# Optimization experiments

Hardware: AMD Instinct MI355X
Metric: run time of the kernel (lower is better)

The kernel has to match this reference:

```python
import jax, jax.numpy as jnp
import numpy as np

B, H, S, D = 4, 16, 2048, 64
NEG = -9e15


def setup_inputs() -> dict:
    key = jax.random.key(0)
    kq, kk, kv = jax.random.split(key, 3)
    q = jax.random.normal(kq, (B, H, S, D), dtype=jnp.float32)
    k = jax.random.normal(kk, (B, H, S, D), dtype=jnp.float32)
    v = jax.random.normal(kv, (B, H, S, D), dtype=jnp.float32)
    # causal mask: 1 where attention allowed, 0 where masked
    mask = jnp.tril(jnp.ones((S, S), dtype=jnp.int32))[None, None]
    return {"q": q, "k": k, "v": v, "mask": mask}


def reference(q, k, v, mask):
    d_k = q.shape[-1]
    # [B,H,S,S] scores
    scores = jnp.einsum("bhqd,bhkd->bhqk", q, k) / jnp.sqrt(jnp.float32(d_k))
    scores = jnp.where(mask == 0, jnp.float32(NEG), scores)
    attn = jax.nn.softmax(scores, axis=-1)
    return jnp.einsum("bhqk,bhkd->bhqd", attn, v)
```

## Files before the change

### kernel.cpp

```cpp
#include <hip/hip_runtime.h>

#define SLEN 2048
#define DH 64
#define NH 64
#define KVB 64
#define NT 32
#define NP 16
#define NEGBIG (-1e30f)
#define SCALE 0.18033688011112042f

typedef __attribute__((ext_vector_type(8))) short bf16x8;
typedef __attribute__((ext_vector_type(8))) unsigned short u16x8;
typedef __attribute__((ext_vector_type(16))) float f32x16;
typedef __attribute__((ext_vector_type(4))) float f32x4;
typedef __attribute__((ext_vector_type(4))) unsigned int u32x4;

__device__ __forceinline__ ushort f2bf(float f) {
  union { float f; unsigned int u; } v; v.f = f;
  unsigned int r = v.u + 0x7fffu + ((v.u >> 16) & 1u);
  return (ushort)(r >> 16);
}

__device__ __forceinline__ unsigned int cvtpk(float lo, float hi2) {
  unsigned int r;
  asm("v_cvt_pk_bf16_f32 %0, %1, %2" : "=v"(r) : "v"(lo), "v"(hi2));
  return r;
}

__device__ __forceinline__ float xsumh(float x) { return x + __shfl_xor(x, 32); }

__device__ __forceinline__ void gload16(const ushort* g, ushort* l) {
  __builtin_amdgcn_global_load_lds(
      (const __attribute__((address_space(1))) void*)g,
      (__attribute__((address_space(3))) void*)l, 16, 0, 0);
}

__global__ __launch_bounds__(256) void prep_k(const float* __restrict__ Kg,
                                              ushort* __restrict__ wsK) {
  const int head = blockIdx.x, tile = blockIdx.y, tid = threadIdx.x;
  const float* src = Kg + ((size_t)head * SLEN + (size_t)tile * KVB) * DH;
  ushort* dst = wsK + ((size_t)head * NT + tile) * (KVB * DH);
#pragma unroll
  for (int i = 0; i < 2; ++i) {
    const int id = tid + i * 256;
    const int r = id >> 3, c = id & 7;
    float4 a = *reinterpret_cast<const float4*>(src + r * DH + c * 8);
    float4 b = *reinterpret_cast<const float4*>(src + r * DH + c * 8 + 4);
    u16x8 t;
    t[0] = f2bf(a.x); t[1] = f2bf(a.y); t[2] = f2bf(a.z); t[3] = f2bf(a.w);
    t[4] = f2bf(b.x); t[5] = f2bf(b.y); t[6] = f2bf(b.z); t[7] = f2bf(b.w);
    *reinterpret_cast<u16x8*>(dst + r * DH + ((c ^ (r & 7)) * 8)) = t;
  }
}

__global__ __launch_bounds__(256) void prep_v(const float* __restrict__ Vg,
                                              ushort* __restrict__ wsV) {
  __shared__ float Vl[KVB][DH + 1];
  const int head = blockIdx.x, tile = blockIdx.y, tid = threadIdx.x;
  const float* src = Vg + ((size_t)head * SLEN + (size_t)tile * KVB) * DH;
#pragma unroll
  for (int i = 0; i < 4; ++i) {
    const int n = tid + i * 256;
    const int row = n >> 4, c4 = (n & 15) << 2;
    *reinterpret_cast<float4*>(&Vl[row][c4]) =
        *reinterpret_cast<const float4*>(src + row * DH + c4);
  }
  __syncthreads();
  ushort* dst = wsV + ((size_t)head * NT + tile) * (KVB * DH);
#pragma unroll
  for (int i = 0; i < 2; ++i) {
    const int id = tid + i * 256;
    const int d = id >> 3, c = id & 7;
    u16x8 t;
#pragma unroll
    for (int j = 0; j < 8; ++j) t[j] = f2bf(Vl[c * 8 + j][d]);
    *reinterpret_cast<u16x8*>(dst + d * DH + ((c ^ (d & 7)) * 8)) = t;
  }
}

__device__ __forceinline__ void qkt(const ushort* __restrict__ Kl,
                                    const bf16x8* qf, f32x16& s0, f32x16& s1,
                                    int ql, int hi) {
  s0 = (f32x16)0.0f; s1 = (f32x16)0.0f;
  __builtin_amdgcn_s_setprio(1);
#pragma unroll
  for (int ks = 0; ks < 4; ++ks) {
    const int c = ((ks * 2 + hi) ^ (ql & 7)) * 8;
    bf16x8 kf0 = *reinterpret_cast<const bf16x8*>(Kl + ql * 64 + c);
    bf16x8 kf1 = *reinterpret_cast<const bf16x8*>(Kl + (32 + ql) * 64 + c);
    s0 = __builtin_amdgcn_mfma_f32_32x32x16_bf16(kf0, qf[ks], s0, 0, 0, 0);
    s1 = __builtin_amdgcn_mfma_f32_32x32x16_bf16(kf1, qf[ks], s1, 0, 0, 0);
  }
  __builtin_amdgcn_s_setprio(0);
}

__device__ __forceinline__ void fin(const ushort* __restrict__ Vl,
                                    f32x16& s0, f32x16& s1, f32x16& o0,
                                    f32x16& o1, f32x4& lv, int t,
                                    int tl, int q0, int ql, int hi) {
  if (t == tl) {
    const int qg = q0 + ql;
#pragma unroll
    for (int r = 0; r < 16; ++r) {
      const int kr = t * 64 + (r & 3) + 8 * (r >> 2) + 4 * hi;
      if (kr > qg)      s0[r] = NEGBIG;
      if (kr + 32 > qg) s1[r] = NEGBIG;
    }
  }

#pragma unroll
  for (int r = 0; r < 16; ++r) s0[r] = __builtin_exp2f(s0[r]);
#pragma unroll
  for (int r = 0; r < 16; ++r) s1[r] = __builtin_exp2f(s1[r]);

#pragma unroll
  for (int r = 0; r < 16; ++r) lv[r & 3] += s0[r] + s1[r];

  unsigned int pw0[8], pw1[8];
#pragma unroll
  for (int g = 0; g < 4; ++g)
#pragma unroll
    for (int j = 0; j < 2; ++j) {
      pw0[g * 2 + j] = cvtpk(s0[4 * g + 2 * j], s0[4 * g + 2 * j + 1]);
      pw1[g * 2 + j] = cvtpk(s1[4 * g + 2 * j], s1[4 * g + 2 * j + 1]);
    }

  __builtin_amdgcn_s_setprio(1);
#pragma unroll
  for (int st = 0; st < 4; ++st) {
    const unsigned int* PW = (st < 2) ? pw0 : pw1;
    const int KH = st & 1;
    const unsigned int a0 = PW[4 * KH + 0], a1 = PW[4 * KH + 1];
    const unsigned int b0 = PW[4 * KH + 2], b1 = PW[4 * KH + 3];
    const unsigned int s0w = hi ? a0 : b0, s1w = hi ? a1 : b1;
    const unsigned int r0 = __shfl_xor(s0w, 32), r1 = __shfl_xor(s1w, 32);
    const unsigned int k0 = hi ? b0 : a0, k1 = hi ? b1 : a1;
    u32x4 fu;
    fu[0] = hi ? r0 : k0; fu[1] = hi ? r1 : k1;
    fu[2] = hi ? k0 : r0; fu[3] = hi ? k1 : r1;
    const bf16x8 pf = __builtin_bit_cast(bf16x8, fu);
    const int cv = ((st * 2 + hi) ^ (ql & 7)) * 8;
    const bf16x8 vf0 = *reinterpret_cast<const bf16x8*>(Vl + ql * 64 + cv);
    const bf16x8 vf1 = *reinterpret_cast<const bf16x8*>(Vl + (32 + ql) * 64 + cv);
    o0 = __builtin_amdgcn_mfma_f32_32x32x16_bf16(vf0, pf, o0, 0, 0, 0);
    o1 = __builtin_amdgcn_mfma_f32_32x32x16_bf16(vf1, pf, o1, 0, 0, 0);
  }
  __builtin_amdgcn_s_setprio(0);
}

__device__ __forceinline__ void load_q(const float* Qh, int q0, int ql, int hi,
                                       bf16x8* qf) {
  const float* qrow = Qh + (size_t)(q0 + ql) * DH;
#pragma unroll
  for (int ks = 0; ks < 4; ++ks) {
    const int d0 = ks * 16 + hi * 8;
    float4 a = *reinterpret_cast<const float4*>(qrow + d0);
    float4 b = *reinterpret_cast<const float4*>(qrow + d0 + 4);
    bf16x8 t;
    t[0] = (short)f2bf(a.x * SCALE); t[1] = (short)f2bf(a.y * SCALE);
    t[2] = (short)f2bf(a.z * SCALE); t[3] = (short)f2bf(a.w * SCALE);
    t[4] = (short)f2bf(b.x * SCALE); t[5] = (short)f2bf(b.y * SCALE);
    t[6] = (short)f2bf(b.z * SCALE); t[7] = (short)f2bf(b.w * SCALE);
    qf[ks] = t;
  }
}

__device__ __forceinline__ void epi(float* Ow, float* Oh, const f32x16& o,
                                    float invl, int q0, int subd, int lane) {
  const int ql = lane & 31, hi = lane >> 5;
#pragma unroll
  for (int g = 0; g < 4; ++g) {
    float4 vv = make_float4(o[4 * g] * invl, o[4 * g + 1] * invl,
                            o[4 * g + 2] * invl, o[4 * g + 3] * invl);
    *reinterpret_cast<float4*>(Ow + ql * 36 + 8 * g + 4 * hi) = vv;
  }
#pragma unroll
  for (int i = 0; i < 4; ++i) {
    const int qr = (lane >> 3) + i * 8;
    const int c4 = (lane & 7) * 4;
    float4 vv = *reinterpret_cast<const float4*>(Ow + qr * 36 + c4);
    *reinterpret_cast<float4*>(Oh + (size_t)(q0 + qr) * DH + subd * 32 + c4) = vv;
  }
}

__global__ __launch_bounds__(128, 2) void attn_fwd7(
    const float* __restrict__ Qg, const ushort* __restrict__ wsK,
    const ushort* __restrict__ wsV, float* __restrict__ Og) {
  __shared__ __align__(16) float smem[8192];
  ushort* stg = (ushort*)smem;

  const int head = blockIdx.x;
  const int p    = blockIdx.y;
  const int tid  = threadIdx.x;
  const int w    = tid >> 6;
  const int lane = tid & 63;
  const int hi   = lane >> 5;
  const int ql   = lane & 31;

  const int q0A = p * 64 + w * 32;
  const int q0B = (31 - p) * 64 + w * 32;
  const int tlA = p;
  const int tlB = 31 - p;
  const int nt  = 32 - p;

  const float*  Qh    = Qg + (size_t)head * SLEN * DH;
  float*        Oh    = Og + (size_t)head * SLEN * DH;
  const ushort* kbase = wsK + (size_t)head * (NT * KVB * DH);
  const ushort* vbase = wsV + (size_t)head * (NT * KVB * DH);

#define STAGE(buf, t)                                                          \
  do {                                                                         \
    const size_t tb_ = (size_t)(t) * 4096;                                     \
    _Pragma("unroll")                                                          \
    for (int j_ = 0; j_ < 4; ++j_) {                                           \
      gload16(kbase + tb_ + j_ * 1024 + tid * 8,                               \
              stg + (buf) * 8192 + j_ * 1024 + tid * 8);                       \
      gload16(vbase + tb_ + j_ * 1024 + tid * 8,                               \
              stg + (buf) * 8192 + 4096 + j_ * 1024 + tid * 8);                \
    }                                                                          \
  } while (0)

  STAGE(0, 0);

  bf16x8 qfA[4], qfB[4];
  load_q(Qh, q0A, ql, hi, qfA);
  load_q(Qh, q0B, ql, hi, qfB);

  f32x16 oA0 = (f32x16)0.0f, oA1 = (f32x16)0.0f;
  f32x16 oB0 = (f32x16)0.0f, oB1 = (f32x16)0.0f;
  f32x4 lvA = (f32x4)0.0f, lvB = (f32x4)0.0f;

  __syncthreads();

  int cur = 0;
  for (int t = 0; t < nt; ++t) {
    if (t + 1 < nt) STAGE(cur ^ 1, t + 1);

    const ushort* Kl = stg + cur * 8192;
    const ushort* Vl = Kl + 4096;
    const bool doA = (t <= tlA);

    f32x16 sB0, sB1, sA0, sA1;
    qkt(Kl, qfB, sB0, sB1, ql, hi);
    if (doA) qkt(Kl, qfA, sA0, sA1, ql, hi);
    fin(Vl, sB0, sB1, oB0, oB1, lvB, t, tlB, q0B, ql, hi);
    if (doA) fin(Vl, sA0, sA1, oA0, oA1, lvA, t, tlA, q0A, ql, hi);

    __syncthreads();
    cur ^= 1;
  }
#undef STAGE

  const float lAs = xsumh(lvA[0] + lvA[1] + lvA[2] + lvA[3]);
  const float lBs = xsumh(lvB[0] + lvB[1] + lvB[2] + lvB[3]);

  float* Ow = smem + w * 1152;
  const float iA = 1.0f / lAs, iB = 1.0f / lBs;
  epi(Ow, Oh, oA0, iA, q0A, 0, lane);
  epi(Ow, Oh, oA1, iA, q0A, 1, lane);
  epi(Ow, Oh, oB0, iB, q0B, 0, lane);
  epi(Ow, Oh, oB1, iB, q0B, 1, lane);
}

extern "C" void kernel_launch(void* const* d_in, const int* in_sizes, int n_in,
                              void* d_out, int out_size, void* d_ws, size_t ws_size,
                              hipStream_t stream) {
  const float* q = (const float*)d_in[0];
  const float* k = (const float*)d_in[1];
  const float* v = (const float*)d_in[2];
  float* out = (float*)d_out;

  const size_t per = (size_t)NH * SLEN * DH;
  ushort* wsK = (ushort*)d_ws;
  ushort* wsV = wsK + per;

  prep_k<<<dim3(NH, NT), 256, 0, stream>>>(k, wsK);
  prep_v<<<dim3(NH, NT), 256, 0, stream>>>(v, wsV);
  attn_fwd7<<<dim3(NH, NP), 128, 0, stream>>>(q, wsK, wsV, out);
}
```

Measured before the change: 91.61 us.

## Split KV tiles across two wave pairs per block and merge partial accumulators

Each block grows from two to four waves. The two wave pairs take alternating KV tiles, so each pair processes half of the causal tile range. This is a split-K style approach. Partial O accumulators and row sums from the second pair are written to shared memory and added into the first pair, which then normalises and writes the output. The software double-buffered prefetch is replaced by loading both tiles and then synchronising, so load and compute no longer overlap inside a block. The merge also adds extra barriers and LDS traffic. Launch bounds change to 256 threads with 3 blocks per SM.

```diff
diff --git a/kernel.cpp b/kernel.cpp
--- a/kernel.cpp
+++ b/kernel.cpp
@@ -8,6 +8,7 @@
 #define NP 16
 #define NEGBIG (-1e30f)
 #define SCALE 0.18033688011112042f
+#define REGION_F 4864
 
 typedef __attribute__((ext_vector_type(8))) short bf16x8;
 typedef __attribute__((ext_vector_type(8))) unsigned short u16x8;
@@ -183,10 +184,10 @@
   }
 }
 
-__global__ __launch_bounds__(128, 2) void attn_fwd7(
+__global__ __launch_bounds__(256, 3) void attn_fwd8(
     const float* __restrict__ Qg, const ushort* __restrict__ wsK,
     const ushort* __restrict__ wsV, float* __restrict__ Og) {
-  __shared__ __align__(16) float smem[8192];
+  __shared__ __align__(16) float smem[2 * REGION_F];
   ushort* stg = (ushort*)smem;
 
   const int head = blockIdx.x;
@@ -196,32 +197,19 @@
   const int lane = tid & 63;
   const int hi   = lane >> 5;
   const int ql   = lane & 31;
-
-  const int q0A = p * 64 + w * 32;
-  const int q0B = (31 - p) * 64 + w * 32;
+  const int sel  = w & 1;
+  const int pw   = w >> 1;
+
+  const int q0A = p * 64 + sel * 32;
+  const int q0B = (31 - p) * 64 + sel * 32;
   const int tlA = p;
   const int tlB = 31 - p;
-  const int nt  = 32 - p;
 
   const float*  Qh    = Qg + (size_t)head * SLEN * DH;
   float*        Oh    = Og + (size_t)head * SLEN * DH;
   const ushort* kbase = wsK + (size_t)head * (NT * KVB * DH);
   const ushort* vbase = wsV + (size_t)head * (NT * KVB * DH);
 
-#define STAGE(buf, t)                                                          \
-  do {                                                                         \
-    const size_t tb_ = (size_t)(t) * 4096;                                     \
-    _Pragma("unroll")                                                          \
-    for (int j_ = 0; j_ < 4; ++j_) {                                           \
-      gload16(kbase + tb_ + j_ * 1024 + tid * 8,                               \
-              stg + (buf) * 8192 + j_ * 1024 + tid * 8);                       \
-      gload16(vbase + tb_ + j_ * 1024 + tid * 8,                               \
-              stg + (buf) * 8192 + 4096 + j_ * 1024 + tid * 8);                \
-    }                                                                          \
-  } while (0)
-
-  STAGE(0, 0);
-
   bf16x8 qfA[4], qfB[4];
   load_q(Qh, q0A, ql, hi, qfA);
   load_q(Qh, q0B, ql, hi, qfB);
@@ -230,36 +218,81 @@
   f32x16 oB0 = (f32x16)0.0f, oB1 = (f32x16)0.0f;
   f32x4 lvA = (f32x4)0.0f, lvB = (f32x4)0.0f;
 
+#define STAGE1(slot, t)                                                        \
+  do {                                                                         \
+    const size_t tb_ = (size_t)(t) * 4096;                                     \
+    gload16(kbase + tb_ + tid * 8,        stg + (slot) * 8192 + tid * 8);      \
+    gload16(kbase + tb_ + 2048 + tid * 8, stg + (slot) * 8192 + 2048 + tid * 8);\
+    gload16(vbase + tb_ + tid * 8,        stg + (slot) * 8192 + 4096 + tid * 8);\
+    gload16(vbase + tb_ + 2048 + tid * 8,                                      \
+            stg + (slot) * 8192 + 6144 + tid * 8);                             \
+  } while (0)
+
+  for (int g = 0; g <= tlB; g += 2) {
+    STAGE1(0, g);
+    if (g + 1 <= tlB) STAGE1(1, g + 1);
+    __syncthreads();
+
+    const int t = g + pw;
+    if (t <= tlB) {
+      const ushort* Kl = stg + pw * 8192;
+      const ushort* Vl = Kl + 4096;
+      const bool doA = (t <= tlA);
+      f32x16 sB0, sB1, sA0, sA1;
+      qkt(Kl, qfB, sB0, sB1, ql, hi);
+      if (doA) qkt(Kl, qfA, sA0, sA1, ql, hi);
+      fin(Vl, sB0, sB1, oB0, oB1, lvB, t, tlB, q0B, ql, hi);
+      if (doA) fin(Vl, sA0, sA1, oA0, oA1, lvA, t, tlA, q0A, ql, hi);
+    }
+    __syncthreads();
+  }
+#undef STAGE1
+
+  if (pw == 1) {
+    float* R = smem + sel * REGION_F;
+#define DUMP(OACC, A)                                                          \
+    _Pragma("unroll")                                                          \
+    for (int g = 0; g < 4; ++g)                                                \
+      *reinterpret_cast<float4*>(R + lane * 68 + (A) * 16 + g * 4) =           \
+          make_float4(OACC[4 * g], OACC[4 * g + 1], OACC[4 * g + 2],           \
+                      OACC[4 * g + 3]);
+    DUMP(oA0, 0); DUMP(oA1, 1); DUMP(oB0, 2); DUMP(oB1, 3);
+#undef DUMP
+    *reinterpret_cast<float4*>(R + 64 * 68 + lane * 8)     =
+        make_float4(lvA[0], lvA[1], lvA[2], lvA[3]);
+    *reinterpret_cast<float4*>(R + 64 * 68 + lane * 8 + 4) =
+        make_float4(lvB[0], lvB[1], lvB[2], lvB[3]);
+  }
   __syncthreads();
-
-  int cur = 0;
-  for (int t = 0; t < nt; ++t) {
-    if (t + 1 < nt) STAGE(cur ^ 1, t + 1);
-
-    const ushort* Kl = stg + cur * 8192;
-    const ushort* Vl = Kl + 4096;
-    const bool doA = (t <= tlA);
-
-    f32x16 sB0, sB1, sA0, sA1;
-    qkt(Kl, qfB, sB0, sB1, ql, hi);
-    if (doA) qkt(Kl, qfA, sA0, sA1, ql, hi);
-    fin(Vl, sB0, sB1, oB0, oB1, lvB, t, tlB, q0B, ql, hi);
-    if (doA) fin(Vl, sA0, sA1, oA0, oA1, lvA, t, tlA, q0A, ql, hi);
-
-    __syncthreads();
-    cur ^= 1;
-  }
-#undef STAGE
-
-  const float lAs = xsumh(lvA[0] + lvA[1] + lvA[2] + lvA[3]);
-  const float lBs = xsumh(lvB[0] + lvB[1] + lvB[2] + lvB[3]);
-
-  float* Ow = smem + w * 1152;
-  const float iA = 1.0f / lAs, iB = 1.0f / lBs;
-  epi(Ow, Oh, oA0, iA, q0A, 0, lane);
-  epi(Ow, Oh, oA1, iA, q0A, 1, lane);
-  epi(Ow, Oh, oB0, iB, q0B, 0, lane);
-  epi(Ow, Oh, oB1, iB, q0B, 1, lane);
+  if (pw == 0) {
+    const float* R = smem + sel * REGION_F;
+#define TAKE(OACC, A)                                                          \
+    _Pragma("unroll")                                                          \
+    for (int g = 0; g < 4; ++g) {                                              \
+      float4 vv = *reinterpret_cast<const float4*>(R + lane * 68 + (A) * 16 +  \
+                                                   g * 4);                     \
+      OACC[4 * g] += vv.x; OACC[4 * g + 1] += vv.y;                            \
+      OACC[4 * g + 2] += vv.z; OACC[4 * g + 3] += vv.w;                        \
+    }
+    TAKE(oA0, 0); TAKE(oA1, 1); TAKE(oB0, 2); TAKE(oB1, 3);
+#undef TAKE
+    float4 la = *reinterpret_cast<const float4*>(R + 64 * 68 + lane * 8);
+    float4 lb = *reinterpret_cast<const float4*>(R + 64 * 68 + lane * 8 + 4);
+    lvA[0] += la.x; lvA[1] += la.y; lvA[2] += la.z; lvA[3] += la.w;
+    lvB[0] += lb.x; lvB[1] += lb.y; lvB[2] += lb.z; lvB[3] += lb.w;
+  }
+  __syncthreads();
+
+  if (pw == 0) {
+    const float lAs = xsumh(lvA[0] + lvA[1] + lvA[2] + lvA[3]);
+    const float lBs = xsumh(lvB[0] + lvB[1] + lvB[2] + lvB[3]);
+    float* Ow = smem + w * 1152;
+    const float iA = 1.0f / lAs, iB = 1.0f / lBs;
+    epi(Ow, Oh, oA0, iA, q0A, 0, lane);
+    epi(Ow, Oh, oA1, iA, q0A, 1, lane);
+    epi(Ow, Oh, oB0, iB, q0B, 0, lane);
+    epi(Ow, Oh, oB1, iB, q0B, 1, lane);
+  }
 }
 
 extern "C" void kernel_launch(void* const* d_in, const int* in_sizes, int n_in,
@@ -276,5 +309,5 @@
 
   prep_k<<<dim3(NH, NT), 256, 0, stream>>>(k, wsK);
   prep_v<<<dim3(NH, NT), 256, 0, stream>>>(v, wsV);
-  attn_fwd7<<<dim3(NH, NP), 128, 0, stream>>>(q, wsK, wsV, out);
-}
+  attn_fwd8<<<dim3(NH, NP), 256, 0, stream>>>(q, wsK, wsV, out);
+}
```

Result: slower. 124.5 us (+36.0%).

## Fuse K/V prep, skip masked diagonal sub-tiles, compute row sums via MFMA

Applied to the files above, without the earlier changes.

Merges the K and V bf16 conversion kernels into one launch to cut a kernel launch. In the attention kernel, wave 0 on the diagonal tile skips the upper 32-key half entirely (QK, exp, pack and PV), and the QK loop shares K fragment loads between the A and B query blocks. Row-sum accumulation moves from per-lane VALU adds plus a cross-half shuffle to an extra MFMA against a ones vector. This adds MFMA work per tile and more live registers, which may reduce occupancy.

```diff
diff --git a/kernel.cpp b/kernel.cpp
--- a/kernel.cpp
+++ b/kernel.cpp
@@ -12,7 +12,6 @@
 typedef __attribute__((ext_vector_type(8))) short bf16x8;
 typedef __attribute__((ext_vector_type(8))) unsigned short u16x8;
 typedef __attribute__((ext_vector_type(16))) float f32x16;
-typedef __attribute__((ext_vector_type(4))) float f32x4;
 typedef __attribute__((ext_vector_type(4))) unsigned int u32x4;
 
 __device__ __forceinline__ ushort f2bf(float f) {
@@ -27,123 +26,129 @@
   return r;
 }
 
-__device__ __forceinline__ float xsumh(float x) { return x + __shfl_xor(x, 32); }
-
 __device__ __forceinline__ void gload16(const ushort* g, ushort* l) {
   __builtin_amdgcn_global_load_lds(
       (const __attribute__((address_space(1))) void*)g,
       (__attribute__((address_space(3))) void*)l, 16, 0, 0);
 }
 
-__global__ __launch_bounds__(256) void prep_k(const float* __restrict__ Kg,
-                                              ushort* __restrict__ wsK) {
+__global__ __launch_bounds__(256) void prep_kv(const float* __restrict__ Kg,
+                                               const float* __restrict__ Vg,
+                                               ushort* __restrict__ wsK,
+                                               ushort* __restrict__ wsV) {
+  __shared__ float Vsh[KVB][DH + 1];
   const int head = blockIdx.x, tile = blockIdx.y, tid = threadIdx.x;
-  const float* src = Kg + ((size_t)head * SLEN + (size_t)tile * KVB) * DH;
-  ushort* dst = wsK + ((size_t)head * NT + tile) * (KVB * DH);
+  const size_t goff = ((size_t)head * SLEN + (size_t)tile * KVB) * DH;
+  const float* srcK = Kg + goff;
+  const float* srcV = Vg + goff;
+  ushort* dstK = wsK + ((size_t)head * NT + tile) * (KVB * DH);
+  ushort* dstV = wsV + ((size_t)head * NT + tile) * (KVB * DH);
 #pragma unroll
   for (int i = 0; i < 2; ++i) {
     const int id = tid + i * 256;
     const int r = id >> 3, c = id & 7;
-    float4 a = *reinterpret_cast<const float4*>(src + r * DH + c * 8);
-    float4 b = *reinterpret_cast<const float4*>(src + r * DH + c * 8 + 4);
+    float4 a = *reinterpret_cast<const float4*>(srcK + r * DH + c * 8);
+    float4 b = *reinterpret_cast<const float4*>(srcK + r * DH + c * 8 + 4);
     u16x8 t;
     t[0] = f2bf(a.x); t[1] = f2bf(a.y); t[2] = f2bf(a.z); t[3] = f2bf(a.w);
     t[4] = f2bf(b.x); t[5] = f2bf(b.y); t[6] = f2bf(b.z); t[7] = f2bf(b.w);
-    *reinterpret_cast<u16x8*>(dst + r * DH + ((c ^ (r & 7)) * 8)) = t;
-  }
-}
-
-__global__ __launch_bounds__(256) void prep_v(const float* __restrict__ Vg,
-                                              ushort* __restrict__ wsV) {
-  __shared__ float Vl[KVB][DH + 1];
-  const int head = blockIdx.x, tile = blockIdx.y, tid = threadIdx.x;
-  const float* src = Vg + ((size_t)head * SLEN + (size_t)tile * KVB) * DH;
+    *reinterpret_cast<u16x8*>(dstK + r * DH + ((c ^ (r & 7)) * 8)) = t;
+  }
 #pragma unroll
   for (int i = 0; i < 4; ++i) {
     const int n = tid + i * 256;
     const int row = n >> 4, c4 = (n & 15) << 2;
-    *reinterpret_cast<float4*>(&Vl[row][c4]) =
-        *reinterpret_cast<const float4*>(src + row * DH + c4);
+    *reinterpret_cast<float4*>(&Vsh[row][c4]) =
+        *reinterpret_cast<const float4*>(srcV + row * DH + c4);
   }
   __syncthreads();
-  ushort* dst = wsV + ((size_t)head * NT + tile) * (KVB * DH);
 #pragma unroll
   for (int i = 0; i < 2; ++i) {
     const int id = tid + i * 256;
     const int d = id >> 3, c = id & 7;
     u16x8 t;
 #pragma unroll
-    for (int j = 0; j < 8; ++j) t[j] = f2bf(Vl[c * 8 + j][d]);
-    *reinterpret_cast<u16x8*>(dst + d * DH + ((c ^ (d & 7)) * 8)) = t;
-  }
-}
-
-__device__ __forceinline__ void qkt(const ushort* __restrict__ Kl,
-                                    const bf16x8* qf, f32x16& s0, f32x16& s1,
-                                    int ql, int hi) {
-  s0 = (f32x16)0.0f; s1 = (f32x16)0.0f;
-  __builtin_amdgcn_s_setprio(1);
-#pragma unroll
-  for (int ks = 0; ks < 4; ++ks) {
-    const int c = ((ks * 2 + hi) ^ (ql & 7)) * 8;
-    bf16x8 kf0 = *reinterpret_cast<const bf16x8*>(Kl + ql * 64 + c);
-    bf16x8 kf1 = *reinterpret_cast<const bf16x8*>(Kl + (32 + ql) * 64 + c);
-    s0 = __builtin_amdgcn_mfma_f32_32x32x16_bf16(kf0, qf[ks], s0, 0, 0, 0);
-    s1 = __builtin_amdgcn_mfma_f32_32x32x16_bf16(kf1, qf[ks], s1, 0, 0, 0);
-  }
-  __builtin_amdgcn_s_setprio(0);
-}
-
-__device__ __forceinline__ void fin(const ushort* __restrict__ Vl,
-                                    f32x16& s0, f32x16& s1, f32x16& o0,
-                                    f32x16& o1, f32x4& lv, int t,
-                                    int tl, int q0, int ql, int hi) {
-  if (t == tl) {
+    for (int j = 0; j < 8; ++j) t[j] = f2bf(Vsh[c * 8 + j][d]);
+    *reinterpret_cast<u16x8*>(dstV + d * DH + ((c ^ (d & 7)) * 8)) = t;
+  }
+}
+
+template <int MODE>
+__device__ __forceinline__ void softmax_pack(f32x16& s0, f32x16& s1,
+                                             unsigned int* pw0,
+                                             unsigned int* pw1, int t, int q0,
+                                             int ql, int hi) {
+  if (MODE == 1) {
     const int qg = q0 + ql;
 #pragma unroll
     for (int r = 0; r < 16; ++r) {
       const int kr = t * 64 + (r & 3) + 8 * (r >> 2) + 4 * hi;
-      if (kr > qg)      s0[r] = NEGBIG;
+      if (kr > qg) s0[r] = NEGBIG;
+    }
+  }
+  if (MODE == 2) {
+    const int qg = q0 + ql;
+#pragma unroll
+    for (int r = 0; r < 16; ++r) {
+      const int kr = t * 64 + (r & 3) + 8 * (r >> 2) + 4 * hi;
       if (kr + 32 > qg) s1[r] = NEGBIG;
     }
   }
-
 #pragma unroll
   for (int r = 0; r < 16; ++r) s0[r] = __builtin_exp2f(s0[r]);
-#pragma unroll
-  for (int r = 0; r < 16; ++r) s1[r] = __builtin_exp2f(s1[r]);
-
-#pragma unroll
-  for (int r = 0; r < 16; ++r) lv[r & 3] += s0[r] + s1[r];
-
-  unsigned int pw0[8], pw1[8];
+  if (MODE != 1) {
+#pragma unroll
+    for (int r = 0; r < 16; ++r) s1[r] = __builtin_exp2f(s1[r]);
+  }
 #pragma unroll
   for (int g = 0; g < 4; ++g)
 #pragma unroll
     for (int j = 0; j < 2; ++j) {
       pw0[g * 2 + j] = cvtpk(s0[4 * g + 2 * j], s0[4 * g + 2 * j + 1]);
-      pw1[g * 2 + j] = cvtpk(s1[4 * g + 2 * j], s1[4 * g + 2 * j + 1]);
-    }
-
+      if (MODE != 1)
+        pw1[g * 2 + j] = cvtpk(s1[4 * g + 2 * j], s1[4 * g + 2 * j + 1]);
+    }
+}
+
+__device__ __forceinline__ bf16x8 xchg(const unsigned int* PW, int KH, int hi) {
+  const unsigned int a0 = PW[4 * KH + 0], a1 = PW[4 * KH + 1];
+  const unsigned int b0 = PW[4 * KH + 2], b1 = PW[4 * KH + 3];
+  const unsigned int s0w = hi ? a0 : b0, s1w = hi ? a1 : b1;
+  const unsigned int r0 = __shfl_xor(s0w, 32), r1 = __shfl_xor(s1w, 32);
+  const unsigned int k0 = hi ? b0 : a0, k1 = hi ? b1 : a1;
+  u32x4 fu;
+  fu[0] = hi ? r0 : k0; fu[1] = hi ? r1 : k1;
+  fu[2] = hi ? k0 : r0; fu[3] = hi ? k1 : r1;
+  return __builtin_bit_cast(bf16x8, fu);
+}
+
+__device__ __forceinline__ void pv_dual(
+    const ushort* __restrict__ Vl, const unsigned int* pwA0,
+    const unsigned int* pwA1, const unsigned int* pwB0,
+    const unsigned int* pwB1, f32x16& oA0, f32x16& oA1, f32x16& lacA,
+    f32x16& oB0, f32x16& oB1, f32x16& lacB, bool doA, bool skipA1,
+    bool skipB1, int ql, int hi, bf16x8 onesf) {
   __builtin_amdgcn_s_setprio(1);
 #pragma unroll
   for (int st = 0; st < 4; ++st) {
-    const unsigned int* PW = (st < 2) ? pw0 : pw1;
-    const int KH = st & 1;
-    const unsigned int a0 = PW[4 * KH + 0], a1 = PW[4 * KH + 1];
-    const unsigned int b0 = PW[4 * KH + 2], b1 = PW[4 * KH + 3];
-    const unsigned int s0w = hi ? a0 : b0, s1w = hi ? a1 : b1;
-    const unsigned int r0 = __shfl_xor(s0w, 32), r1 = __shfl_xor(s1w, 32);
-    const unsigned int k0 = hi ? b0 : a0, k1 = hi ? b1 : a1;
-    u32x4 fu;
-    fu[0] = hi ? r0 : k0; fu[1] = hi ? r1 : k1;
-    fu[2] = hi ? k0 : r0; fu[3] = hi ? k1 : r1;
-    const bf16x8 pf = __builtin_bit_cast(bf16x8, fu);
+    const bool bAct = !(skipB1 && st >= 2);
+    const bool aAct = doA && !(skipA1 && st >= 2);
+    if (!aAct && !bAct) continue;
     const int cv = ((st * 2 + hi) ^ (ql & 7)) * 8;
     const bf16x8 vf0 = *reinterpret_cast<const bf16x8*>(Vl + ql * 64 + cv);
     const bf16x8 vf1 = *reinterpret_cast<const bf16x8*>(Vl + (32 + ql) * 64 + cv);
-    o0 = __builtin_amdgcn_mfma_f32_32x32x16_bf16(vf0, pf, o0, 0, 0, 0);
-    o1 = __builtin_amdgcn_mfma_f32_32x32x16_bf16(vf1, pf, o1, 0, 0, 0);
+    if (bAct) {
+      const bf16x8 pf = xchg(st < 2 ? pwB0 : pwB1, st & 1, hi);
+      oB0 = __builtin_amdgcn_mfma_f32_32x32x16_bf16(vf0, pf, oB0, 0, 0, 0);
+      oB1 = __builtin_amdgcn_mfma_f32_32x32x16_bf16(vf1, pf, oB1, 0, 0, 0);
+      lacB = __builtin_amdgcn_mfma_f32_32x32x16_bf16(onesf, pf, lacB, 0, 0, 0);
+    }
+    if (aAct) {
+      const bf16x8 pf = xchg(st < 2 ? pwA0 : pwA1, st & 1, hi);
+      oA0 = __builtin_amdgcn_mfma_f32_32x32x16_bf16(vf0, pf, oA0, 0, 0, 0);
+      oA1 = __builtin_amdgcn_mfma_f32_32x32x16_bf16(vf1, pf, oA1, 0, 0, 0);
+      lacA = __builtin_amdgcn_mfma_f32_32x32x16_bf16(onesf, pf, lacA, 0, 0, 0);
+    }
   }
   __builtin_amdgcn_s_setprio(0);
 }
@@ -183,7 +188,7 @@
   }
 }
 
-__global__ __launch_bounds__(128, 2) void attn_fwd7(
+__global__ __launch_bounds__(128, 2) void attn_fwd10(
     const float* __restrict__ Qg, const ushort* __restrict__ wsK,
     const ushort* __restrict__ wsV, float* __restrict__ Og) {
   __shared__ __align__(16) float smem[8192];
@@ -202,6 +207,7 @@
   const int tlA = p;
   const int tlB = 31 - p;
   const int nt  = 32 - p;
+  const bool lower = (w == 0);
 
   const float*  Qh    = Qg + (size_t)head * SLEN * DH;
   float*        Oh    = Og + (size_t)head * SLEN * DH;
@@ -226,9 +232,12 @@
   load_q(Qh, q0A, ql, hi, qfA);
   load_q(Qh, q0B, ql, hi, qfB);
 
-  f32x16 oA0 = (f32x16)0.0f, oA1 = (f32x16)0.0f;
-  f32x16 oB0 = (f32x16)0.0f, oB1 = (f32x16)0.0f;
-  f32x4 lvA = (f32x4)0.0f, lvB = (f32x4)0.0f;
+  bf16x8 onesf;
+#pragma unroll
+  for (int j = 0; j < 8; ++j) onesf[j] = (short)0x3F80;
+
+  f32x16 oA0 = (f32x16)0.0f, oA1 = (f32x16)0.0f, lacA = (f32x16)0.0f;
+  f32x16 oB0 = (f32x16)0.0f, oB1 = (f32x16)0.0f, lacB = (f32x16)0.0f;
 
   __syncthreads();
 
@@ -238,21 +247,60 @@
 
     const ushort* Kl = stg + cur * 8192;
     const ushort* Vl = Kl + 4096;
-    const bool doA = (t <= tlA);
-
-    f32x16 sB0, sB1, sA0, sA1;
-    qkt(Kl, qfB, sB0, sB1, ql, hi);
-    if (doA) qkt(Kl, qfA, sA0, sA1, ql, hi);
-    fin(Vl, sB0, sB1, oB0, oB1, lvB, t, tlB, q0B, ql, hi);
-    if (doA) fin(Vl, sA0, sA1, oA0, oA1, lvA, t, tlA, q0A, ql, hi);
+    const bool doA   = (t <= tlA);
+    const bool diagA = (t == tlA);
+    const bool diagB = (t == tlB);
+
+    f32x16 sA0 = (f32x16)0.0f, sA1 = (f32x16)0.0f;
+    f32x16 sB0 = (f32x16)0.0f, sB1 = (f32x16)0.0f;
+    const bool needK1 = !(diagB && lower);
+    const bool doA1   = doA && !(diagA && lower);
+    __builtin_amdgcn_s_setprio(1);
+#pragma unroll
+    for (int ks = 0; ks < 4; ++ks) {
+      const int c = ((ks * 2 + hi) ^ (ql & 7)) * 8;
+      const bf16x8 kf0 = *reinterpret_cast<const bf16x8*>(Kl + ql * 64 + c);
+      sB0 = __builtin_amdgcn_mfma_f32_32x32x16_bf16(kf0, qfB[ks], sB0, 0, 0, 0);
+      if (doA)
+        sA0 = __builtin_amdgcn_mfma_f32_32x32x16_bf16(kf0, qfA[ks], sA0, 0, 0, 0);
+      if (needK1) {
+        const bf16x8 kf1 =
+            *reinterpret_cast<const bf16x8*>(Kl + (32 + ql) * 64 + c);
+        sB1 = __builtin_amdgcn_mfma_f32_32x32x16_bf16(kf1, qfB[ks], sB1, 0, 0, 0);
+        if (doA1)
+          sA1 = __builtin_amdgcn_mfma_f32_32x32x16_bf16(kf1, qfA[ks], sA1, 0, 0, 0);
+      }
+    }
+    __builtin_amdgcn_s_setprio(0);
+
+    unsigned int pwA0[8], pwA1[8], pwB0[8], pwB1[8];
+    const bool skipB1 = diagB && lower;
+    const bool skipA1 = diagA && lower;
+    if (diagB) {
+      if (lower) softmax_pack<1>(sB0, sB1, pwB0, pwB1, t, q0B, ql, hi);
+      else       softmax_pack<2>(sB0, sB1, pwB0, pwB1, t, q0B, ql, hi);
+    } else {
+      softmax_pack<0>(sB0, sB1, pwB0, pwB1, t, q0B, ql, hi);
+    }
+    if (doA) {
+      if (diagA) {
+        if (lower) softmax_pack<1>(sA0, sA1, pwA0, pwA1, t, q0A, ql, hi);
+        else       softmax_pack<2>(sA0, sA1, pwA0, pwA1, t, q0A, ql, hi);
+      } else {
+        softmax_pack<0>(sA0, sA1, pwA0, pwA1, t, q0A, ql, hi);
+      }
+    }
+
+    pv_dual(Vl, pwA0, pwA1, pwB0, pwB1, oA0, oA1, lacA, oB0, oB1, lacB, doA,
+            skipA1, skipB1, ql, hi, onesf);
 
     __syncthreads();
     cur ^= 1;
   }
 #undef STAGE
 
-  const float lAs = xsumh(lvA[0] + lvA[1] + lvA[2] + lvA[3]);
-  const float lBs = xsumh(lvB[0] + lvB[1] + lvB[2] + lvB[3]);
+  const float lAs = lacA[0];
+  const float lBs = lacB[0];
 
   float* Ow = smem + w * 1152;
   const float iA = 1.0f / lAs, iB = 1.0f / lBs;
@@ -274,7 +322,6 @@
   ushort* wsK = (ushort*)d_ws;
   ushort* wsV = wsK + per;
 
-  prep_k<<<dim3(NH, NT), 256, 0, stream>>>(k, wsK);
-  prep_v<<<dim3(NH, NT), 256, 0, stream>>>(v, wsV);
-  attn_fwd7<<<dim3(NH, NP), 128, 0, stream>>>(q, wsK, wsV, out);
-}
+  prep_kv<<<dim3(NH, NT), 256, 0, stream>>>(k, v, wsK, wsV);
+  attn_fwd10<<<dim3(NH, NP), 128, 0, stream>>>(q, wsK, wsV, out);
+}
```

New measurement: 102.4 us. +11.7%, slower.

## Split paired query tiles across four waves and fuse K/V prep kernels

Applied to the files above, without the earlier changes.

The attention kernel now uses 256 threads with four waves, each owning one 32-row query block instead of two waves each handling both the early and late tiles. Waves whose causal range is already done skip compute but still take part in staging and barriers. This doubles wave-level parallelism and cuts per-wave registers, at the cost of idle waves on the short-tile half. The separate K and V conversion kernels are also merged into one launch to remove a launch.

```diff
diff --git a/kernel.cpp b/kernel.cpp
--- a/kernel.cpp
+++ b/kernel.cpp
@@ -35,46 +35,44 @@
       (__attribute__((address_space(3))) void*)l, 16, 0, 0);
 }
 
-__global__ __launch_bounds__(256) void prep_k(const float* __restrict__ Kg,
-                                              ushort* __restrict__ wsK) {
+__global__ __launch_bounds__(256) void prep_kv(const float* __restrict__ Kg,
+                                               const float* __restrict__ Vg,
+                                               ushort* __restrict__ wsK,
+                                               ushort* __restrict__ wsV) {
+  __shared__ float Vsh[KVB][DH + 1];
   const int head = blockIdx.x, tile = blockIdx.y, tid = threadIdx.x;
-  const float* src = Kg + ((size_t)head * SLEN + (size_t)tile * KVB) * DH;
-  ushort* dst = wsK + ((size_t)head * NT + tile) * (KVB * DH);
+  const size_t goff = ((size_t)head * SLEN + (size_t)tile * KVB) * DH;
+  const float* srcK = Kg + goff;
+  const float* srcV = Vg + goff;
+  ushort* dstK = wsK + ((size_t)head * NT + tile) * (KVB * DH);
+  ushort* dstV = wsV + ((size_t)head * NT + tile) * (KVB * DH);
 #pragma unroll
   for (int i = 0; i < 2; ++i) {
     const int id = tid + i * 256;
     const int r = id >> 3, c = id & 7;
-    float4 a = *reinterpret_cast<const float4*>(src + r * DH + c * 8);
-    float4 b = *reinterpret_cast<const float4*>(src + r * DH + c * 8 + 4);
+    float4 a = *reinterpret_cast<const float4*>(srcK + r * DH + c * 8);
+    float4 b = *reinterpret_cast<const float4*>(srcK + r * DH + c * 8 + 4);
     u16x8 t;
     t[0] = f2bf(a.x); t[1] = f2bf(a.y); t[2] = f2bf(a.z); t[3] = f2bf(a.w);
     t[4] = f2bf(b.x); t[5] = f2bf(b.y); t[6] = f2bf(b.z); t[7] = f2bf(b.w);
-    *reinterpret_cast<u16x8*>(dst + r * DH + ((c ^ (r & 7)) * 8)) = t;
-  }
-}
-
-__global__ __launch_bounds__(256) void prep_v(const float* __restrict__ Vg,
-                                              ushort* __restrict__ wsV) {
-  __shared__ float Vl[KVB][DH + 1];
-  const int head = blockIdx.x, tile = blockIdx.y, tid = threadIdx.x;
-  const float* src = Vg + ((size_t)head * SLEN + (size_t)tile * KVB) * DH;
+    *reinterpret_cast<u16x8*>(dstK + r * DH + ((c ^ (r & 7)) * 8)) = t;
+  }
 #pragma unroll
   for (int i = 0; i < 4; ++i) {
     const int n = tid + i * 256;
     const int row = n >> 4, c4 = (n & 15) << 2;
-    *reinterpret_cast<float4*>(&Vl[row][c4]) =
-        *reinterpret_cast<const float4*>(src + row * DH + c4);
+    *reinterpret_cast<float4*>(&Vsh[row][c4]) =
+        *reinterpret_cast<const float4*>(srcV + row * DH + c4);
   }
   __syncthreads();
-  ushort* dst = wsV + ((size_t)head * NT + tile) * (KVB * DH);
 #pragma unroll
   for (int i = 0; i < 2; ++i) {
     const int id = tid + i * 256;
     const int d = id >> 3, c = id & 7;
     u16x8 t;
 #pragma unroll
-    for (int j = 0; j < 8; ++j) t[j] = f2bf(Vl[c * 8 + j][d]);
-    *reinterpret_cast<u16x8*>(dst + d * DH + ((c ^ (d & 7)) * 8)) = t;
+    for (int j = 0; j < 8; ++j) t[j] = f2bf(Vsh[c * 8 + j][d]);
+    *reinterpret_cast<u16x8*>(dstV + d * DH + ((c ^ (d & 7)) * 8)) = t;
   }
 }
 
@@ -107,12 +105,10 @@
       if (kr + 32 > qg) s1[r] = NEGBIG;
     }
   }
-
 #pragma unroll
   for (int r = 0; r < 16; ++r) s0[r] = __builtin_exp2f(s0[r]);
 #pragma unroll
   for (int r = 0; r < 16; ++r) s1[r] = __builtin_exp2f(s1[r]);
-
 #pragma unroll
   for (int r = 0; r < 16; ++r) lv[r & 3] += s0[r] + s1[r];
 
@@ -183,7 +179,7 @@
   }
 }
 
-__global__ __launch_bounds__(128, 2) void attn_fwd7(
+__global__ __launch_bounds__(256, 4) void attn_fwd12(
     const float* __restrict__ Qg, const ushort* __restrict__ wsK,
     const ushort* __restrict__ wsV, float* __restrict__ Og) {
   __shared__ __align__(16) float smem[8192];
@@ -196,12 +192,12 @@
   const int lane = tid & 63;
   const int hi   = lane >> 5;
   const int ql   = lane & 31;
-
-  const int q0A = p * 64 + w * 32;
-  const int q0B = (31 - p) * 64 + w * 32;
-  const int tlA = p;
-  const int tlB = 31 - p;
-  const int nt  = 32 - p;
+  const int sel   = w & 1;
+  const int which = w >> 1;
+
+  const int q0 = (which ? (31 - p) : p) * 64 + sel * 32;
+  const int tl = q0 >> 6;
+  const int nt = 32 - p;
 
   const float*  Qh    = Qg + (size_t)head * SLEN * DH;
   float*        Oh    = Og + (size_t)head * SLEN * DH;
@@ -212,23 +208,21 @@
   do {                                                                         \
     const size_t tb_ = (size_t)(t) * 4096;                                     \
     _Pragma("unroll")                                                          \
-    for (int j_ = 0; j_ < 4; ++j_) {                                           \
-      gload16(kbase + tb_ + j_ * 1024 + tid * 8,                               \
-              stg + (buf) * 8192 + j_ * 1024 + tid * 8);                       \
-      gload16(vbase + tb_ + j_ * 1024 + tid * 8,                               \
-              stg + (buf) * 8192 + 4096 + j_ * 1024 + tid * 8);                \
+    for (int j_ = 0; j_ < 2; ++j_) {                                           \
+      gload16(kbase + tb_ + j_ * 2048 + tid * 8,                               \
+              stg + (buf) * 8192 + j_ * 2048 + tid * 8);                       \
+      gload16(vbase + tb_ + j_ * 2048 + tid * 8,                               \
+              stg + (buf) * 8192 + 4096 + j_ * 2048 + tid * 8);                \
     }                                                                          \
   } while (0)
 
   STAGE(0, 0);
 
-  bf16x8 qfA[4], qfB[4];
-  load_q(Qh, q0A, ql, hi, qfA);
-  load_q(Qh, q0B, ql, hi, qfB);
-
-  f32x16 oA0 = (f32x16)0.0f, oA1 = (f32x16)0.0f;
-  f32x16 oB0 = (f32x16)0.0f, oB1 = (f32x16)0.0f;
-  f32x4 lvA = (f32x4)0.0f, lvB = (f32x4)0.0f;
+  bf16x8 qf[4];
+  load_q(Qh, q0, ql, hi, qf);
+
+  f32x16 o0 = (f32x16)0.0f, o1 = (f32x16)0.0f;
+  f32x4 lv = (f32x4)0.0f;
 
   __syncthreads();
 
@@ -236,30 +230,24 @@
   for (int t = 0; t < nt; ++t) {
     if (t + 1 < nt) STAGE(cur ^ 1, t + 1);
 
-    const ushort* Kl = stg + cur * 8192;
-    const ushort* Vl = Kl + 4096;
-    const bool doA = (t <= tlA);
-
-    f32x16 sB0, sB1, sA0, sA1;
-    qkt(Kl, qfB, sB0, sB1, ql, hi);
-    if (doA) qkt(Kl, qfA, sA0, sA1, ql, hi);
-    fin(Vl, sB0, sB1, oB0, oB1, lvB, t, tlB, q0B, ql, hi);
-    if (doA) fin(Vl, sA0, sA1, oA0, oA1, lvA, t, tlA, q0A, ql, hi);
-
+    if (t <= tl) {
+      const ushort* Kl = stg + cur * 8192;
+      const ushort* Vl = Kl + 4096;
+      f32x16 s0, s1;
+      qkt(Kl, qf, s0, s1, ql, hi);
+      fin(Vl, s0, s1, o0, o1, lv, t, tl, q0, ql, hi);
+    }
     __syncthreads();
     cur ^= 1;
   }
 #undef STAGE
 
-  const float lAs = xsumh(lvA[0] + lvA[1] + lvA[2] + lvA[3]);
-  const float lBs = xsumh(lvB[0] + lvB[1] + lvB[2] + lvB[3]);
+  const float ls = xsumh(lv[0] + lv[1] + lv[2] + lv[3]);
 
   float* Ow = smem + w * 1152;
-  const float iA = 1.0f / lAs, iB = 1.0f / lBs;
-  epi(Ow, Oh, oA0, iA, q0A, 0, lane);
-  epi(Ow, Oh, oA1, iA, q0A, 1, lane);
-  epi(Ow, Oh, oB0, iB, q0B, 0, lane);
-  epi(Ow, Oh, oB1, iB, q0B, 1, lane);
+  const float il = 1.0f / ls;
+  epi(Ow, Oh, o0, il, q0, 0, lane);
+  epi(Ow, Oh, o1, il, q0, 1, lane);
 }
 
 extern "C" void kernel_launch(void* const* d_in, const int* in_sizes, int n_in,
@@ -274,7 +262,6 @@
   ushort* wsK = (ushort*)d_ws;
   ushort* wsV = wsK + per;
 
-  prep_k<<<dim3(NH, NT), 256, 0, stream>>>(k, wsK);
-  prep_v<<<dim3(NH, NT), 256, 0, stream>>>(v, wsV);
-  attn_fwd7<<<dim3(NH, NP), 128, 0, stream>>>(q, wsK, wsV, out);
-}
+  prep_kv<<<dim3(NH, NT), 256, 0, stream>>>(k, v, wsK, wsV);
+  attn_fwd12<<<dim3(NH, NP), 256, 0, stream>>>(q, wsK, wsV, out);
+}
```

New measurement: 95.74 us. 1.05x slower.
